# Kernel tuning notes

Measured on AMD Instinct MI355X. Metric: run time of the kernel, lower is better.

Reference implementation:

```python
import jax, jax.numpy as jnp
import numpy as np

B, M, S, D, Q, H = 8, 8192, 128, 512, 32, 8
HD = D // H
LN_EPS = 1e-5


def setup_inputs() -> dict:
    key = jax.random.key(0)
    ks = jax.random.split(key, 12)
    inp = {
        "memory": jax.random.normal(ks[0], (B, M, D), dtype=jnp.float32),
        "context": jax.random.normal(ks[1], (B, S, D), dtype=jnp.float32),
        "memory_mask": jax.random.randint(ks[2], (B, M), 0, 2).astype(bool),
        # learned parameters
        "queries_param": jax.random.normal(ks[3], (Q, D), dtype=jnp.float32) * 0.02,
        "ctx_w": jax.random.normal(ks[4], (D, D), dtype=jnp.float32) / np.sqrt(D),
        "ctx_b": jnp.zeros((D,), dtype=jnp.float32),
        "in_w": jax.random.normal(ks[5], (3 * D, D), dtype=jnp.float32) / np.sqrt(D),
        "in_b": jnp.zeros((3 * D,), dtype=jnp.float32),
        "out_w": jax.random.normal(ks[6], (D, D), dtype=jnp.float32) / np.sqrt(D),
        "out_b": jnp.zeros((D,), dtype=jnp.float32),
        "ln_g": jnp.ones((D,), dtype=jnp.float32),
        "ln_b": jnp.zeros((D,), dtype=jnp.float32),
        "gate_w": jax.random.normal(ks[7], (Q, D), dtype=jnp.float32) / np.sqrt(D),
        "gate_b": jnp.zeros((Q,), dtype=jnp.float32),
    }
    return inp


def _forward(memory, context, memory_mask, queries_param, ctx_w, ctx_b,
             in_w, in_b, out_w, out_b, ln_g, ln_b, gate_w, gate_b):
    b = memory.shape[0]
    # pool context over sequence dim (rank-3 path)
    pooled = context.mean(axis=1)  # [B, D]
    # queries + projected context
    queries = queries_param[None, :, :] + (pooled @ ctx_w.T + ctx_b)[:, None, :]  # [B, Q, D]
    # MultiheadAttention in-projection
    wq, wk, wv = in_w[:D], in_w[D:2 * D], in_w[2 * D:]
    bq, bk, bv = in_b[:D], in_b[D:2 * D], in_b[2 * D:]
    qh = (queries @ wq.T + bq).reshape(b, Q, H, HD).transpose(0, 2, 1, 3)   # [B,H,Q,hd]
    kh = (memory @ wk.T + bk).reshape(b, M, H, HD).transpose(0, 2, 1, 3)    # [B,H,M,hd]
    vh = (memory @ wv.T + bv).reshape(b, M, H, HD).transpose(0, 2, 1, 3)    # [B,H,M,hd]
    scale = 1.0 / np.sqrt(HD)
    scores = jnp.einsum('bhqd,bhkd->bhqk', qh * scale, kh)                  # [B,H,Q,M]
    # key_padding_mask: True in memory_mask means valid; invalid -> -inf
    scores = jnp.where(memory_mask[:, None, None, :], scores, -jnp.inf)
    attn = jax.nn.softmax(scores, axis=-1)                                   # [B,H,Q,M]
    ctx_out = jnp.einsum('bhqk,bhkd->bhqd', attn, vh)
    ctx_out = ctx_out.transpose(0, 2, 1, 3).reshape(b, Q, D)
    readouts = ctx_out @ out_w.T + out_b                                     # [B,Q,D]
    attention = attn.mean(axis=1)                                            # [B,Q,M]
    gates = jax.nn.sigmoid(pooled @ gate_w.T + gate_b)                       # [B,Q]
    readouts = readouts * gates[:, :, None]
    mu = readouts.mean(axis=-1, keepdims=True)
    var = readouts.var(axis=-1, keepdims=True)
    readouts_norm = (readouts - mu) * jax.lax.rsqrt(var + LN_EPS) * ln_g + ln_b
    return readouts_norm, attention, gates, queries


def reference(memory, context, memory_mask, queries_param, ctx_w, ctx_b,
              in_w, in_b, out_w, out_b, ln_g, ln_b, gate_w, gate_b):
    return _forward(memory, context, memory_mask, queries_param, ctx_w, ctx_b,
                    in_w, in_b, out_w, out_b, ln_g, ln_b, gate_w, gate_b)
```

## Files before the change

### kernel.cpp

```cpp
#include <hip/hip_runtime.h>
#include <cstdint>

#define BB 8
#define MM 8192
#define SS 128
#define DD 512
#define QQ 32
#define HH 8
#define HDD 64
#define LN_EPS 1e-5f

typedef __bf16 bf16;
typedef __attribute__((ext_vector_type(8))) __bf16 bf16x8;
typedef __attribute__((ext_vector_type(4))) __bf16 bf16x4;
typedef __attribute__((ext_vector_type(4))) float f32x4;

__global__ void k_pooled(const float* __restrict__ ctx, float* __restrict__ pooled) {
    int b = blockIdx.x, d = threadIdx.x;
    const float* p = ctx + (size_t)b * SS * DD + d;
    float s = 0.f;
#pragma unroll 8
    for (int i = 0; i < SS; i++) s += p[(size_t)i * DD];
    pooled[b * DD + d] = s * (1.0f / SS);
}

__global__ void k_qproj(const float* __restrict__ pooled, const float* __restrict__ ctx_w,
                        const float* __restrict__ ctx_b, const float* __restrict__ qp,
                        float* __restrict__ q_out) {
    __shared__ float pl[DD];
    int b = blockIdx.x, t = threadIdx.x;
    pl[t] = pooled[b * DD + t];
    __syncthreads();
    const f32x4* wr = (const f32x4*)(ctx_w + (size_t)t * DD);
    const f32x4* pv = (const f32x4*)pl;
    float acc = 0.f;
#pragma unroll 8
    for (int k = 0; k < DD / 4; k++) {
        f32x4 w = wr[k], p = pv[k];
        acc += w.x * p.x + w.y * p.y + w.z * p.z + w.w * p.w;
    }
    float proj = acc + ctx_b[t];
#pragma unroll 4
    for (int q = 0; q < QQ; q++)
        q_out[((size_t)b * QQ + q) * DD + t] = qp[q * DD + t] + proj;
}

__global__ void k_gates(const float* __restrict__ pooled, const float* __restrict__ gate_w,
                        const float* __restrict__ gate_b, float* __restrict__ gates_out) {
    int bq = blockIdx.x;
    int b = bq >> 5, q = bq & 31, l = threadIdx.x;
    const f32x4* pv = (const f32x4*)(pooled + b * DD);
    const f32x4* wv = (const f32x4*)(gate_w + q * DD);
    float acc = 0.f;
    for (int k = l; k < DD / 4; k += 64) {
        f32x4 p = pv[k], w = wv[k];
        acc += p.x * w.x + p.y * w.y + p.z * w.z + p.w * w.w;
    }
    for (int off = 32; off; off >>= 1) acc += __shfl_xor(acc, off, 64);
    if (l == 0) gates_out[bq] = 1.0f / (1.0f + __expf(-(acc + gate_b[q])));
}

__global__ void k_qh(const float* __restrict__ q_in, const float* __restrict__ in_w,
                     const float* __restrict__ in_b, float* __restrict__ qh) {
    __shared__ float qr[DD];
    int bq = blockIdx.x, t = threadIdx.x;
    qr[t] = q_in[(size_t)bq * DD + t];
    qr[t + 256] = q_in[(size_t)bq * DD + t + 256];
    __syncthreads();
    const f32x4* qv = (const f32x4*)qr;
#pragma unroll
    for (int jj = 0; jj < 2; jj++) {
        int j = t + jj * 256;
        const f32x4* wv = (const f32x4*)(in_w + (size_t)j * DD);
        float acc = 0.f;
#pragma unroll 8
        for (int k = 0; k < DD / 4; k++) {
            f32x4 w = wv[k], p = qv[k];
            acc += w.x * p.x + w.y * p.y + w.z * p.z + w.w * p.w;
        }
        qh[(size_t)bq * DD + j] = 0.125f * (acc + in_b[j]);
    }
}

__global__ void k_cvt(const float* __restrict__ src, bf16* __restrict__ dst, int n4) {
    int i = blockIdx.x * blockDim.x + threadIdx.x;
    if (i >= n4) return;
    f32x4 v = ((const f32x4*)src)[i];
    bf16x4 o;
    o.x = (bf16)v.x; o.y = (bf16)v.y; o.z = (bf16)v.z; o.w = (bf16)v.w;
    ((bf16x4*)dst)[i] = o;
}

__global__ __launch_bounds__(256) void k_gemm_kv(const bf16* __restrict__ A,
                                                 const bf16* __restrict__ Bw,
                                                 const float* __restrict__ in_b,
                                                 bf16* __restrict__ kvK,
                                                 bf16* __restrict__ Vt) {
    __shared__ bf16 sm[2 * 128 * 64];
    bf16* As = sm;
    bf16* Bs = sm + 128 * 64;
    int tid = threadIdx.x;
    int w = tid >> 6, l = tid & 63;
    int bm = blockIdx.x >> 3, bn = blockIdx.x & 7;
    int wm = w >> 1, wn = w & 1;
    const f32x4 vzero = {0.f, 0.f, 0.f, 0.f};
    f32x4 acc[4][4];
#pragma unroll
    for (int i = 0; i < 4; i++)
#pragma unroll
        for (int j = 0; j < 4; j++) acc[i][j] = vzero;

    int lr = l >> 3;
    int lc = (l & 7) * 8;
    const bf16* Ag = A + (size_t)(bm * 128) * DD;
    const bf16* Bg = Bw + (size_t)(bn * 128) * DD;
    int lq = l & 15, quad = l >> 4;

    for (int k0 = 0; k0 < DD; k0 += 64) {
        __syncthreads();
#pragma unroll
        for (int i = 0; i < 4; i++) {
            int seg = w * 4 + i;
            const bf16* ga = Ag + (size_t)(seg * 8 + lr) * DD + k0 + lc;
            const bf16* gb = Bg + (size_t)(seg * 8 + lr) * DD + k0 + lc;
            __builtin_amdgcn_global_load_lds((const __attribute__((address_space(1))) void*)ga,
                                             (__attribute__((address_space(3))) void*)(As + seg * 512),
                                             16, 0, 0);
            __builtin_amdgcn_global_load_lds((const __attribute__((address_space(1))) void*)gb,
                                             (__attribute__((address_space(3))) void*)(Bs + seg * 512),
                                             16, 0, 0);
        }
        __syncthreads();
#pragma unroll
        for (int ks = 0; ks < 64; ks += 32) {
            bf16x8 af[4], bfr[4];
#pragma unroll
            for (int i = 0; i < 4; i++)
                af[i] = *(const bf16x8*)(As + (wm * 64 + i * 16 + lq) * 64 + ks + quad * 8);
#pragma unroll
            for (int j = 0; j < 4; j++)
                bfr[j] = *(const bf16x8*)(Bs + (wn * 64 + j * 16 + lq) * 64 + ks + quad * 8);
#pragma unroll
            for (int i = 0; i < 4; i++)
#pragma unroll
                for (int j = 0; j < 4; j++)
                    acc[i][j] = __builtin_amdgcn_mfma_f32_16x16x32_bf16(af[i], bfr[j], acc[i][j], 0, 0, 0);
        }
    }
    if (bn < 4) {
#pragma unroll
        for (int j = 0; j < 4; j++) {
            int c = bn * 128 + wn * 64 + j * 16 + lq;
            float bias = in_b[512 + c];
#pragma unroll
            for (int i = 0; i < 4; i++) {
                int rbase = bm * 128 + wm * 64 + i * 16 + quad * 4;
#pragma unroll
                for (int t = 0; t < 4; t++)
                    kvK[(size_t)(rbase + t) * 512 + c] = (bf16)(acc[i][j][t] + bias);
            }
        }
    } else {
#pragma unroll
        for (int j = 0; j < 4; j++) {
            int c = bn * 128 + wn * 64 + j * 16 + lq;
            float bias = in_b[512 + c];
            int hd = c - 512;
#pragma unroll
            for (int i = 0; i < 4; i++) {
                int rbase = bm * 128 + wm * 64 + i * 16 + quad * 4;
                int b = rbase >> 13, mb = rbase & 8191;
                bf16x4 pk;
#pragma unroll
                for (int t = 0; t < 4; t++) pk[t] = (bf16)(acc[i][j][t] + bias);
                *(bf16x4*)(Vt + ((size_t)(b * 512 + hd)) * MM + mb) = pk;
            }
        }
    }
}

__global__ __launch_bounds__(256) void k_scores(const float* __restrict__ qh,
                                                const bf16* __restrict__ kvK,
                                                const int* __restrict__ mask,
                                                float* __restrict__ scores) {
    int blk = blockIdx.x;
    int mt = blk & 15, h = (blk >> 4) & 7, b = blk >> 7;
    int tid = threadIdx.x, w = tid >> 6, l = tid & 63;
    int lq = l & 15, quad = l >> 4;
    int mbase = mt * 512 + w * 128;

    bf16x8 af[2][2];
#pragma unroll
    for (int i = 0; i < 2; i++)
#pragma unroll
        for (int s = 0; s < 2; s++) {
            const float* qp = qh + ((size_t)(b * QQ + i * 16 + lq)) * DD + h * 64 + s * 32 + quad * 8;
            f32x4 q0 = *(const f32x4*)qp;
            f32x4 q1 = *(const f32x4*)(qp + 4);
            bf16x8 v;
            v[0] = (bf16)q0.x; v[1] = (bf16)q0.y; v[2] = (bf16)q0.z; v[3] = (bf16)q0.w;
            v[4] = (bf16)q1.x; v[5] = (bf16)q1.y; v[6] = (bf16)q1.z; v[7] = (bf16)q1.w;
            af[i][s] = v;
        }

    const f32x4 vzero = {0.f, 0.f, 0.f, 0.f};
    f32x4 acc[2][8];
#pragma unroll
    for (int i = 0; i < 2; i++)
#pragma unroll
        for (int n = 0; n < 8; n++) acc[i][n] = vzero;

#pragma unroll
    for (int n = 0; n < 8; n++) {
        int m = mbase + n * 16 + lq;
        const bf16* kp = kvK + ((size_t)(b * MM + m)) * 512 + h * 64 + quad * 8;
        bf16x8 b0 = *(const bf16x8*)kp;
        bf16x8 b1 = *(const bf16x8*)(kp + 32);
#pragma unroll
        for (int i = 0; i < 2; i++) {
            acc[i][n] = __builtin_amdgcn_mfma_f32_16x16x32_bf16(af[i][0], b0, acc[i][n], 0, 0, 0);
            acc[i][n] = __builtin_amdgcn_mfma_f32_16x16x32_bf16(af[i][1], b1, acc[i][n], 0, 0, 0);
        }
    }
#pragma unroll
    for (int n = 0; n < 8; n++) {
        int m = mbase + n * 16 + lq;
        int mv = mask[b * MM + m];
        float ninf = -__builtin_inff();
#pragma unroll
        for (int i = 0; i < 2; i++)
#pragma unroll
            for (int t = 0; t < 4; t++) {
                int q = i * 16 + quad * 4 + t;
                float val = mv ? acc[i][n][t] : ninf;
                scores[((size_t)(b * HH + h) * QQ + q) * MM + m] = val;
            }
    }
}

__global__ __launch_bounds__(1024) void k_softmax(float* __restrict__ scores,
                                                  float* __restrict__ attn_out) {
    __shared__ float sred[16];
    int bq = blockIdx.x;
    int b = bq >> 5, q = bq & 31;
    int t = threadIdx.x, wid = t >> 6;
    float am[8];
#pragma unroll
    for (int i = 0; i < 8; i++) am[i] = 0.f;

    for (int h = 0; h < HH; h++) {
        float* row = scores + ((size_t)(b * HH + h) * QQ + q) * MM;
        bf16* prow = (bf16*)row;
        float x[8];
#pragma unroll
        for (int i = 0; i < 8; i++) x[i] = row[t + i * 1024];
        float mx = -__builtin_inff();
#pragma unroll
        for (int i = 0; i < 8; i++) mx = fmaxf(mx, x[i]);
        for (int off = 32; off; off >>= 1) mx = fmaxf(mx, __shfl_xor(mx, off, 64));
        if ((t & 63) == 0) sred[wid] = mx;
        __syncthreads();
#pragma unroll
        for (int i = 0; i < 16; i++) mx = fmaxf(mx, sred[i]);
        __syncthreads();
        float sum = 0.f;
#pragma unroll
        for (int i = 0; i < 8; i++) {
            x[i] = __expf(x[i] - mx);
            sum += x[i];
        }
        for (int off = 32; off; off >>= 1) sum += __shfl_xor(sum, off, 64);
        if ((t & 63) == 0) sred[wid] = sum;
        __syncthreads();
        float tot = 0.f;
#pragma unroll
        for (int i = 0; i < 16; i++) tot += sred[i];
        float inv = 1.0f / tot;
#pragma unroll
        for (int i = 0; i < 8; i++) {
            float p = x[i] * inv;
            prow[t + i * 1024] = (bf16)p;
            am[i] += p;
        }
        __syncthreads();
    }
    float* ao = attn_out + (size_t)bq * MM;
#pragma unroll
    for (int i = 0; i < 8; i++) ao[t + i * 1024] = am[i] * (1.0f / HH);
}

__global__ __launch_bounds__(256) void k_pv(const bf16* __restrict__ Pb,
                                            const bf16* __restrict__ Vt,
                                            float* __restrict__ ctxo_p) {
    __shared__ float ctile[QQ * HDD];
    int blk = blockIdx.x;
    int ck = blk & 7, h = (blk >> 3) & 7, b = blk >> 6;
    int t = threadIdx.x, w = t >> 6, l = t & 63;
    int lq = l & 15, quad = l >> 4;
    int m0 = ck * 1024 + w * 256;

    const bf16* Prow0 = Pb + ((size_t)((b * HH + h) * QQ + lq)) * 16384 + m0 + quad * 8;
    const bf16* Prow1 = Prow0 + (size_t)16 * 16384;
    const bf16* Vrow = Vt + ((size_t)((b * HH + h) * HDD + lq)) * MM + m0 + quad * 8;

    const f32x4 vzero = {0.f, 0.f, 0.f, 0.f};
    f32x4 acc[2][4];
#pragma unroll
    for (int i = 0; i < 2; i++)
#pragma unroll
        for (int j = 0; j < 4; j++) acc[i][j] = vzero;

#pragma unroll 2
    for (int ks = 0; ks < 256; ks += 32) {
        bf16x8 a0 = *(const bf16x8*)(Prow0 + ks);
        bf16x8 a1 = *(const bf16x8*)(Prow1 + ks);
        bf16x8 bv[4];
#pragma unroll
        for (int j = 0; j < 4; j++) bv[j] = *(const bf16x8*)(Vrow + (size_t)j * 16 * MM + ks);
#pragma unroll
        for (int j = 0; j < 4; j++) {
            acc[0][j] = __builtin_amdgcn_mfma_f32_16x16x32_bf16(a0, bv[j], acc[0][j], 0, 0, 0);
            acc[1][j] = __builtin_amdgcn_mfma_f32_16x16x32_bf16(a1, bv[j], acc[1][j], 0, 0, 0);
        }
    }
    for (int i = t; i < QQ * HDD; i += 256) ctile[i] = 0.f;
    __syncthreads();
#pragma unroll
    for (int i = 0; i < 2; i++)
#pragma unroll
        for (int j = 0; j < 4; j++)
#pragma unroll
            for (int tt = 0; tt < 4; tt++) {
                int q = i * 16 + quad * 4 + tt;
                int d = j * 16 + lq;
                atomicAdd(&ctile[q * HDD + d], acc[i][j][tt]);
            }
    __syncthreads();
    float* dst = ctxo_p + (size_t)ck * (BB * QQ * DD);
    for (int i = t; i < QQ * HDD; i += 256) {
        int q = i >> 6, d = i & 63;
        dst[((size_t)(b * QQ + q)) * DD + h * HDD + d] = ctile[i];
    }
}

__global__ __launch_bounds__(256) void k_outln(const float* __restrict__ ctxo_p,
                                               const float* __restrict__ out_w,
                                               const float* __restrict__ out_b,
                                               const float* __restrict__ gates,
                                               const float* __restrict__ ln_g,
                                               const float* __restrict__ ln_b,
                                               float* __restrict__ out0) {
    __shared__ float cr[DD];
    __shared__ float sred[4], sred2[4];
    int bq = blockIdx.x, t = threadIdx.x;
    float c0 = 0.f, c1 = 0.f;
#pragma unroll
    for (int c = 0; c < 8; c++) {
        const float* src = ctxo_p + (size_t)c * (BB * QQ * DD) + (size_t)bq * DD;
        c0 += src[t];
        c1 += src[t + 256];
    }
    cr[t] = c0;
    cr[t + 256] = c1;
    __syncthreads();
    float g = gates[bq];
    const f32x4* cv = (const f32x4*)cr;
    float r[2];
#pragma unroll
    for (int jj = 0; jj < 2; jj++) {
        int j = t + jj * 256;
        const f32x4* wv = (const f32x4*)(out_w + (size_t)j * DD);
        float acc = 0.f;
#pragma unroll 4
        for (int k = 0; k < DD / 4; k++) {
            f32x4 wq = wv[k], cq = cv[k];
            acc += wq.x * cq.x + wq.y * cq.y + wq.z * cq.z + wq.w * cq.w;
        }
        r[jj] = (acc + out_b[j]) * g;
    }
    float s1 = r[0] + r[1];
    float s2 = r[0] * r[0] + r[1] * r[1];
    for (int off = 32; off; off >>= 1) {
        s1 += __shfl_xor(s1, off, 64);
        s2 += __shfl_xor(s2, off, 64);
    }
    int wid = t >> 6;
    if ((t & 63) == 0) { sred[wid] = s1; sred2[wid] = s2; }
    __syncthreads();
    float S1 = sred[0] + sred[1] + sred[2] + sred[3];
    float S2 = sred2[0] + sred2[1] + sred2[2] + sred2[3];
    float mu = S1 * (1.0f / DD);
    float var = S2 * (1.0f / DD) - mu * mu;
    float rs = rsqrtf(var + LN_EPS);
#pragma unroll
    for (int jj = 0; jj < 2; jj++) {
        int j = t + jj * 256;
        out0[(size_t)bq * DD + j] = (r[jj] - mu) * rs * ln_g[j] + ln_b[j];
    }
}

extern "C" void kernel_launch(void* const* d_in, const int* in_sizes, int n_in,
                              void* d_out, int out_size, void* d_ws, size_t ws_size,
                              hipStream_t stream) {
    const float* memory  = (const float*)d_in[0];
    const float* context = (const float*)d_in[1];
    const int*   mask    = (const int*)d_in[2];
    const float* qp      = (const float*)d_in[3];
    const float* ctx_w   = (const float*)d_in[4];
    const float* ctx_b   = (const float*)d_in[5];
    const float* in_w    = (const float*)d_in[6];
    const float* in_b    = (const float*)d_in[7];
    const float* out_w   = (const float*)d_in[8];
    const float* out_b   = (const float*)d_in[9];
    const float* ln_g    = (const float*)d_in[10];
    const float* ln_b    = (const float*)d_in[11];
    const float* gate_w  = (const float*)d_in[12];
    const float* gate_b  = (const float*)d_in[13];

    float* out       = (float*)d_out;
    float* out_ln    = out;
    float* out_attn  = out + 131072;
    float* out_gates = out + 131072 + 2097152;
    float* out_q     = out_gates + 256;

    char* ws = (char*)d_ws;
    bf16*  memB   = (bf16*)ws;
    float* scores = (float*)ws;
    bf16*  Pb     = (bf16*)ws;
    bf16*  kvK    = (bf16*)(ws + 67108864);
    bf16*  Vt     = (bf16*)(ws + 134217728);
    bf16*  kvwB   = (bf16*)(ws + 201326592);
    float* qh     = (float*)(ws + 202375168);
    float* ctxo_p = (float*)(ws + 202899456);
    float* pooled = (float*)(ws + 207093760);

    k_pooled<<<BB, 512, 0, stream>>>(context, pooled);
    k_qproj<<<BB, 512, 0, stream>>>(pooled, ctx_w, ctx_b, qp, out_q);
    k_gates<<<BB * QQ, 64, 0, stream>>>(pooled, gate_w, gate_b, out_gates);
    k_qh<<<BB * QQ, 256, 0, stream>>>(out_q, in_w, in_b, qh);
    k_cvt<<<32768, 256, 0, stream>>>(memory, memB, 8388608);
    k_cvt<<<512, 256, 0, stream>>>(in_w + 262144, kvwB, 131072);
    k_gemm_kv<<<4096, 256, 0, stream>>>(memB, kvwB, in_b, kvK, Vt);
    k_scores<<<1024, 256, 0, stream>>>(qh, kvK, mask, scores);
    k_softmax<<<BB * QQ, 1024, 0, stream>>>(scores, out_attn);
    k_pv<<<BB * HH * 8, 256, 0, stream>>>(Pb, Vt, ctxo_p);
    k_outln<<<BB * QQ, 256, 0, stream>>>(ctxo_p, out_w, out_b, out_gates, ln_g, ln_b, out_ln);
}
```

Baseline: 556.0 us.

## Restructure KV GEMM with swizzled LDS, 512 threads, staged coalesced stores; fuse front kernels

Fuses the pooling, query-projection and gate kernels into a single front kernel, which saves two launches and the round trip of the pooled vector through global memory. The K/V projection GEMM moves to 512 threads per block, with each wave owning a 32x64 sub-tile. LDS loads use an XOR swizzle to avoid bank conflicts, and block indices are remapped so tiles that share operands are scheduled near each other. The epilogue stages results through LDS so K rows and the transposed V are written as 16-byte coalesced stores rather than scattered 2-byte and 8-byte writes, at the cost of extra barriers and LDS traffic.

```diff
diff --git a/kernel.cpp b/kernel.cpp
--- a/kernel.cpp
+++ b/kernel.cpp
@@ -15,49 +15,44 @@
 typedef __attribute__((ext_vector_type(4))) __bf16 bf16x4;
 typedef __attribute__((ext_vector_type(4))) float f32x4;
 
-__global__ void k_pooled(const float* __restrict__ ctx, float* __restrict__ pooled) {
-    int b = blockIdx.x, d = threadIdx.x;
-    const float* p = ctx + (size_t)b * SS * DD + d;
+__global__ __launch_bounds__(512) void k_front(const float* __restrict__ ctx,
+                                               const float* __restrict__ ctx_w,
+                                               const float* __restrict__ ctx_b,
+                                               const float* __restrict__ qp,
+                                               const float* __restrict__ gate_w,
+                                               const float* __restrict__ gate_b,
+                                               float* __restrict__ q_out,
+                                               float* __restrict__ gates_out) {
+    __shared__ float pl[DD];
+    int b = blockIdx.x, t = threadIdx.x;
+    const float* p = ctx + (size_t)b * SS * DD + t;
     float s = 0.f;
 #pragma unroll 8
     for (int i = 0; i < SS; i++) s += p[(size_t)i * DD];
-    pooled[b * DD + d] = s * (1.0f / SS);
-}
-
-__global__ void k_qproj(const float* __restrict__ pooled, const float* __restrict__ ctx_w,
-                        const float* __restrict__ ctx_b, const float* __restrict__ qp,
-                        float* __restrict__ q_out) {
-    __shared__ float pl[DD];
-    int b = blockIdx.x, t = threadIdx.x;
-    pl[t] = pooled[b * DD + t];
+    pl[t] = s * (1.0f / SS);
     __syncthreads();
     const f32x4* wr = (const f32x4*)(ctx_w + (size_t)t * DD);
     const f32x4* pv = (const f32x4*)pl;
     float acc = 0.f;
 #pragma unroll 8
     for (int k = 0; k < DD / 4; k++) {
-        f32x4 w = wr[k], p = pv[k];
-        acc += w.x * p.x + w.y * p.y + w.z * p.z + w.w * p.w;
+        f32x4 w = wr[k], pp = pv[k];
+        acc += w.x * pp.x + w.y * pp.y + w.z * pp.z + w.w * pp.w;
     }
     float proj = acc + ctx_b[t];
 #pragma unroll 4
     for (int q = 0; q < QQ; q++)
         q_out[((size_t)b * QQ + q) * DD + t] = qp[q * DD + t] + proj;
-}
-
-__global__ void k_gates(const float* __restrict__ pooled, const float* __restrict__ gate_w,
-                        const float* __restrict__ gate_b, float* __restrict__ gates_out) {
-    int bq = blockIdx.x;
-    int b = bq >> 5, q = bq & 31, l = threadIdx.x;
-    const f32x4* pv = (const f32x4*)(pooled + b * DD);
-    const f32x4* wv = (const f32x4*)(gate_w + q * DD);
-    float acc = 0.f;
-    for (int k = l; k < DD / 4; k += 64) {
-        f32x4 p = pv[k], w = wv[k];
-        acc += p.x * w.x + p.y * w.y + p.z * w.z + p.w * w.w;
-    }
-    for (int off = 32; off; off >>= 1) acc += __shfl_xor(acc, off, 64);
-    if (l == 0) gates_out[bq] = 1.0f / (1.0f + __expf(-(acc + gate_b[q])));
+    if (t < QQ) {
+        const f32x4* gw = (const f32x4*)(gate_w + (size_t)t * DD);
+        float ga = 0.f;
+#pragma unroll 8
+        for (int k = 0; k < DD / 4; k++) {
+            f32x4 w = gw[k], pp = pv[k];
+            ga += w.x * pp.x + w.y * pp.y + w.z * pp.z + w.w * pp.w;
+        }
+        gates_out[b * QQ + t] = 1.0f / (1.0f + __expf(-(ga + gate_b[t])));
+    }
 }
 
 __global__ void k_qh(const float* __restrict__ q_in, const float* __restrict__ in_w,
@@ -91,38 +86,40 @@
     ((bf16x4*)dst)[i] = o;
 }
 
-__global__ __launch_bounds__(256) void k_gemm_kv(const bf16* __restrict__ A,
+__global__ __launch_bounds__(512) void k_gemm_kv(const bf16* __restrict__ A,
                                                  const bf16* __restrict__ Bw,
                                                  const float* __restrict__ in_b,
                                                  bf16* __restrict__ kvK,
                                                  bf16* __restrict__ Vt) {
-    __shared__ bf16 sm[2 * 128 * 64];
+    __shared__ __align__(16) bf16 sm[2 * 128 * 64];
     bf16* As = sm;
     bf16* Bs = sm + 128 * 64;
     int tid = threadIdx.x;
     int w = tid >> 6, l = tid & 63;
-    int bm = blockIdx.x >> 3, bn = blockIdx.x & 7;
+    int bid = blockIdx.x;
+    int bn = (bid >> 3) & 7;
+    int bm = ((bid >> 6) << 3) | (bid & 7);
     int wm = w >> 1, wn = w & 1;
     const f32x4 vzero = {0.f, 0.f, 0.f, 0.f};
-    f32x4 acc[4][4];
-#pragma unroll
-    for (int i = 0; i < 4; i++)
+    f32x4 acc[2][4];
+#pragma unroll
+    for (int i = 0; i < 2; i++)
 #pragma unroll
         for (int j = 0; j < 4; j++) acc[i][j] = vzero;
 
     int lr = l >> 3;
-    int lc = (l & 7) * 8;
+    int gc = (l & 7) ^ lr;
     const bf16* Ag = A + (size_t)(bm * 128) * DD;
     const bf16* Bg = Bw + (size_t)(bn * 128) * DD;
-    int lq = l & 15, quad = l >> 4;
+    int lq = l & 15, quad = l >> 4, lx = lq & 7;
 
     for (int k0 = 0; k0 < DD; k0 += 64) {
         __syncthreads();
 #pragma unroll
-        for (int i = 0; i < 4; i++) {
-            int seg = w * 4 + i;
-            const bf16* ga = Ag + (size_t)(seg * 8 + lr) * DD + k0 + lc;
-            const bf16* gb = Bg + (size_t)(seg * 8 + lr) * DD + k0 + lc;
+        for (int i = 0; i < 2; i++) {
+            int seg = w * 2 + i;
+            const bf16* ga = Ag + (size_t)(seg * 8 + lr) * DD + k0 + gc * 8;
+            const bf16* gb = Bg + (size_t)(seg * 8 + lr) * DD + k0 + gc * 8;
             __builtin_amdgcn_global_load_lds((const __attribute__((address_space(1))) void*)ga,
                                              (__attribute__((address_space(3))) void*)(As + seg * 512),
                                              16, 0, 0);
@@ -132,49 +129,71 @@
         }
         __syncthreads();
 #pragma unroll
-        for (int ks = 0; ks < 64; ks += 32) {
-            bf16x8 af[4], bfr[4];
-#pragma unroll
-            for (int i = 0; i < 4; i++)
-                af[i] = *(const bf16x8*)(As + (wm * 64 + i * 16 + lq) * 64 + ks + quad * 8);
+        for (int kc = 0; kc < 8; kc += 4) {
+            int ch = (quad + kc) ^ lx;
+            bf16x8 af[2], bfr[4];
+#pragma unroll
+            for (int i = 0; i < 2; i++)
+                af[i] = *(const bf16x8*)(As + (wm * 32 + i * 16 + lq) * 64 + ch * 8);
 #pragma unroll
             for (int j = 0; j < 4; j++)
-                bfr[j] = *(const bf16x8*)(Bs + (wn * 64 + j * 16 + lq) * 64 + ks + quad * 8);
-#pragma unroll
-            for (int i = 0; i < 4; i++)
+                bfr[j] = *(const bf16x8*)(Bs + (wn * 64 + j * 16 + lq) * 64 + ch * 8);
+#pragma unroll
+            for (int i = 0; i < 2; i++)
 #pragma unroll
                 for (int j = 0; j < 4; j++)
                     acc[i][j] = __builtin_amdgcn_mfma_f32_16x16x32_bf16(af[i], bfr[j], acc[i][j], 0, 0, 0);
         }
     }
+
+    __syncthreads();
+    bf16* tile = sm;
     if (bn < 4) {
 #pragma unroll
         for (int j = 0; j < 4; j++) {
-            int c = bn * 128 + wn * 64 + j * 16 + lq;
-            float bias = in_b[512 + c];
-#pragma unroll
-            for (int i = 0; i < 4; i++) {
-                int rbase = bm * 128 + wm * 64 + i * 16 + quad * 4;
-#pragma unroll
-                for (int t = 0; t < 4; t++)
-                    kvK[(size_t)(rbase + t) * 512 + c] = (bf16)(acc[i][j][t] + bias);
+            int col = wn * 64 + j * 16 + lq;
+            float bias = in_b[512 + bn * 128 + col];
+            int cc = col >> 3, cl = col & 7;
+#pragma unroll
+            for (int i = 0; i < 2; i++) {
+                int rbase = wm * 32 + i * 16 + quad * 4;
+#pragma unroll
+                for (int t = 0; t < 4; t++) {
+                    int row = rbase + t;
+                    tile[row * 128 + ((cc ^ (row & 15)) << 3) + cl] = (bf16)(acc[i][j][t] + bias);
+                }
             }
         }
+        __syncthreads();
+        for (int idx = tid; idx < 2048; idx += 512) {
+            int row = idx >> 4, ch2 = idx & 15;
+            bf16x8 v = *(const bf16x8*)(tile + row * 128 + ((ch2 ^ (row & 15)) << 3));
+            *(bf16x8*)(kvK + (size_t)(bm * 128 + row) * 512 + bn * 128 + ch2 * 8) = v;
+        }
     } else {
 #pragma unroll
         for (int j = 0; j < 4; j++) {
-            int c = bn * 128 + wn * 64 + j * 16 + lq;
-            float bias = in_b[512 + c];
-            int hd = c - 512;
-#pragma unroll
-            for (int i = 0; i < 4; i++) {
-                int rbase = bm * 128 + wm * 64 + i * 16 + quad * 4;
-                int b = rbase >> 13, mb = rbase & 8191;
-                bf16x4 pk;
-#pragma unroll
-                for (int t = 0; t < 4; t++) pk[t] = (bf16)(acc[i][j][t] + bias);
-                *(bf16x4*)(Vt + ((size_t)(b * 512 + hd)) * MM + mb) = pk;
+            int col = wn * 64 + j * 16 + lq;
+            float bias = in_b[512 + bn * 128 + col];
+            int cs = col & 15;
+#pragma unroll
+            for (int i = 0; i < 2; i++) {
+                int rbase = wm * 32 + i * 16 + quad * 4;
+#pragma unroll
+                for (int t = 0; t < 4; t++) {
+                    int row = rbase + t;
+                    tile[col * 128 + (((row >> 3) ^ cs) << 3) + (row & 7)] = (bf16)(acc[i][j][t] + bias);
+                }
             }
+        }
+        __syncthreads();
+        int b = bm >> 6;
+        int m0 = (bm & 63) * 128;
+        int hd0 = (bn - 4) * 128;
+        for (int idx = tid; idx < 2048; idx += 512) {
+            int col = idx >> 4, ch2 = idx & 15;
+            bf16x8 v = *(const bf16x8*)(tile + col * 128 + ((ch2 ^ (col & 15)) << 3));
+            *(bf16x8*)(Vt + ((size_t)(b * 512 + hd0 + col)) * MM + m0 + ch2 * 8) = v;
         }
     }
 }
@@ -432,15 +451,12 @@
     bf16*  kvwB   = (bf16*)(ws + 201326592);
     float* qh     = (float*)(ws + 202375168);
     float* ctxo_p = (float*)(ws + 202899456);
-    float* pooled = (float*)(ws + 207093760);
-
-    k_pooled<<<BB, 512, 0, stream>>>(context, pooled);
-    k_qproj<<<BB, 512, 0, stream>>>(pooled, ctx_w, ctx_b, qp, out_q);
-    k_gates<<<BB * QQ, 64, 0, stream>>>(pooled, gate_w, gate_b, out_gates);
+
+    k_front<<<BB, 512, 0, stream>>>(context, ctx_w, ctx_b, qp, gate_w, gate_b, out_q, out_gates);
     k_qh<<<BB * QQ, 256, 0, stream>>>(out_q, in_w, in_b, qh);
     k_cvt<<<32768, 256, 0, stream>>>(memory, memB, 8388608);
     k_cvt<<<512, 256, 0, stream>>>(in_w + 262144, kvwB, 131072);
-    k_gemm_kv<<<4096, 256, 0, stream>>>(memB, kvwB, in_b, kvK, Vt);
+    k_gemm_kv<<<4096, 512, 0, stream>>>(memB, kvwB, in_b, kvK, Vt);
     k_scores<<<1024, 256, 0, stream>>>(qh, kvK, mask, scores);
     k_softmax<<<BB * QQ, 1024, 0, stream>>>(scores, out_attn);
     k_pv<<<BB * HH * 8, 256, 0, stream>>>(Pb, Vt, ctxo_p);
```

Result: faster. 507.1 us (-8.8%).
